# Kernel tuning notes

Measured on AMD Instinct MI355X. Metric: run time of the kernel, lower is better.

Reference implementation:

```python
import jax, jax.numpy as jnp
import numpy as np

N_NODES = 50000
N_EDGES = 800000
IN_F, HID_F, OUT_F = 256, 128, 64


def setup_inputs() -> dict:
    key = jax.random.key(0)
    ks = jax.random.split(key, 9)
    glorot = lambda k, shp: jax.random.normal(k, shp, jnp.float32) * np.sqrt(2.0 / (shp[0] + shp[1]))
    return {
        "x": jax.random.normal(ks[0], (N_NODES, IN_F), jnp.float32),
        "W1": glorot(ks[1], (IN_F, HID_F)),
        "b1": jnp.zeros((HID_F,), jnp.float32),
        "W2": glorot(ks[2], (HID_F, OUT_F)),
        "b2": jnp.zeros((OUT_F,), jnp.float32),
        "Wf": glorot(ks[3], (OUT_F, 2)),
        "bf": jnp.zeros((2,), jnp.float32),
        "src": jax.random.randint(ks[4], (N_EDGES,), 0, N_NODES, jnp.int32),
        "dst": jax.random.randint(ks[5], (N_EDGES,), 0, N_NODES, jnp.int32),
    }


def _gcn_layer(x, src, dst, W, b):
    # DGL GraphConv, norm='both': h = D_in^{-1/2} A D_out^{-1/2} (x W) + b
    n = x.shape[0]
    ones = jnp.ones((src.shape[0],), x.dtype)
    deg_out = jnp.clip(jax.ops.segment_sum(ones, src, num_segments=n), 1.0)
    deg_in = jnp.clip(jax.ops.segment_sum(ones, dst, num_segments=n), 1.0)
    h = x @ W  # transform first (in_feats >= out_feats), cheaper messages
    h = h * jax.lax.rsqrt(deg_out)[:, None]
    agg = jax.ops.segment_sum(h[src], dst, num_segments=n)  # [N, F] sparse aggregate
    return agg * jax.lax.rsqrt(deg_in)[:, None] + b


def reference(x, W1, b1, W2, b2, Wf, bf, src, dst):
    h1 = jax.nn.relu(_gcn_layer(x, src, dst, W1, b1))
    hidden = _gcn_layer(h1, src, dst, W2, b2)
    logits = hidden @ Wf + bf
    return (logits, hidden)
```

## Files before the change

### kernel.cpp

```cpp
#include <hip/hip_runtime.h>
#include <hip/hip_bf16.h>
#include <cstdint>
#include <cstddef>

#define NNODES 50000
#define NEDGES 800000
#define NCH    256
#define CHUNK1 3136
#define NBUCK  196
#define GB1    782
#define SHB    64
#define SHE    12500
#define SHEV   (SHE / 1024)
#define PBN    256
#define PBR    196

typedef unsigned short u16;
typedef unsigned int u32;
typedef short bfrag8 __attribute__((ext_vector_type(8)));
typedef float f32x4 __attribute__((ext_vector_type(4)));

__device__ __forceinline__ u16 f2bf(float f) {
    union { float f; uint32_t i; } v; v.f = f;
    uint32_t r = (v.i + 0x7FFFu + ((v.i >> 16) & 1u)) >> 16;
    return (u16)r;
}
__device__ __forceinline__ float bflo(u32 p) { union { uint32_t i; float f; } v; v.i = p << 16; return v.f; }
__device__ __forceinline__ float bfhi(u32 p) { union { uint32_t i; float f; } v; v.i = p & 0xFFFF0000u; return v.f; }

__global__ __launch_bounds__(256) void pre_kernel(const float* __restrict__ W1, const float* __restrict__ W2,
                                                  u16* __restrict__ P1, u16* __restrict__ P2,
                                                  const int* __restrict__ src, const int* __restrict__ dst,
                                                  u32* __restrict__ histS, u32* __restrict__ histD,
                                                  u32* __restrict__ gh1, int nE) {
    __shared__ u32 hh[12500];
    int b = blockIdx.x, t = threadIdx.x;
    if (b < 2 * SHB) {
        const int* col = (b < SHB) ? src : dst;
        int bb = (b < SHB) ? b : b - SHB;
        for (int j = t; j < 12500; j += 256) hh[j] = 0;
        __syncthreads();
        int beg = bb * SHE;
        const uint4* col4 = (const uint4*)(col + beg);
        #pragma unroll 4
        for (int k = 0; k < SHEV; k++) {
            uint4 e = col4[k * 256 + t];
            atomicAdd(&hh[e.x >> 2], 1u << ((e.x & 3) * 8));
            atomicAdd(&hh[e.y >> 2], 1u << ((e.y & 3) * 8));
            atomicAdd(&hh[e.z >> 2], 1u << ((e.z & 3) * 8));
            atomicAdd(&hh[e.w >> 2], 1u << ((e.w & 3) * 8));
        }
        for (int i = beg + SHEV * 1024 + t; i < beg + SHE; i += 256) {
            u32 n = (u32)col[i];
            atomicAdd(&hh[n >> 2], 1u << ((n & 3) * 8));
        }
        __syncthreads();
        u32* out = ((b < SHB) ? histS : histD) + (size_t)bb * 12500;
        for (int j = t; j < 12500; j += 256) out[j] = hh[j];
    } else if (b < 2 * SHB + NCH) {
        int c = b - 2 * SHB;
        hh[t] = 0;
        __syncthreads();
        int beg = c * CHUNK1, end = min(beg + CHUNK1, nE);
        const uint4* d4 = (const uint4*)(dst + beg);
        int n4 = (end - beg) >> 2;
        for (int k = t; k < n4; k += 256) {
            uint4 e = d4[k];
            atomicAdd(&hh[e.x >> 8], 1u);
            atomicAdd(&hh[e.y >> 8], 1u);
            atomicAdd(&hh[e.z >> 8], 1u);
            atomicAdd(&hh[e.w >> 8], 1u);
        }
        __syncthreads();
        gh1[t * NCH + c] = hh[t];
    } else {
        int i = (b - 2 * SHB - NCH) * 256 + t;
        if (i < 256 * 128) {
            int k = i >> 7, n = i & 127;
            P1[((((k >> 3) << 7) + n) << 3) | (k & 7)] = f2bf(W1[i]);
        }
        if (i < 128 * 64) {
            int k = i >> 6, n = i & 63;
            P2[((((k >> 3) << 6) + n) << 3) | (k & 7)] = f2bf(W2[i]);
        }
    }
}

__global__ __launch_bounds__(256) void red_scan1(const u32* __restrict__ histS, const u32* __restrict__ histD,
                                                 int* __restrict__ deg_out, int* __restrict__ deg_in,
                                                 const u32* __restrict__ gh1, int* __restrict__ scan1,
                                                 int* __restrict__ part1, int* __restrict__ gdh) {
    int t = threadIdx.x, b = blockIdx.x;
    __shared__ int sd[256];
    __shared__ int cnt64[64];
    if (t < 64) cnt64[t] = 0;
    int gi = b * NCH + t;
    int v = (int)gh1[gi];
    sd[t] = v;
    __syncthreads();
    #pragma unroll
    for (int o = 1; o < 256; o <<= 1) {
        int add = (t >= o) ? sd[t - o] : 0;
        __syncthreads();
        sd[t] += add;
        __syncthreads();
    }
    scan1[gi] = sd[t];
    if (t == 255) part1[b] = sd[255];
    int n = b * PBR + t;
    if (t < PBR && n < NNODES) {
        int w = n >> 2, sh = (n & 3) * 8;
        int so = 0, si = 0;
        #pragma unroll 8
        for (int r = 0; r < SHB; r++) {
            so += (int)((histS[(size_t)r * 12500 + w] >> sh) & 255u);
            si += (int)((histD[(size_t)r * 12500 + w] >> sh) & 255u);
        }
        deg_out[n] = so;
        deg_in[n] = si;
        atomicAdd(&cnt64[si > 63 ? 63 : si], 1);
    }
    __syncthreads();
    if (t < 64) gdh[b * 64 + t] = cnt64[t];
}

__global__ __launch_bounds__(256) void scatter1(const int* __restrict__ dst, const int* __restrict__ src,
                                                const u32* __restrict__ gh1, const int* __restrict__ scan1,
                                                const int* __restrict__ part1, u32* __restrict__ sbuf,
                                                const int* __restrict__ gdh, int* __restrict__ gbase, int nE) {
    int t = threadIdx.x, c = blockIdx.x;
    if (c == NCH) {
        __shared__ int colsum[64];
        if (t < 64) {
            int s = 0;
            for (int pb = 0; pb < PBN; pb++) s += gdh[pb * 64 + t];
            colsum[t] = s;
        }
        __syncthreads();
        if (t == 0) {
            int s = 0;
            for (int d = 0; d < 64; d++) { int c0 = colsum[d]; colsum[d] = s; s += c0; }
        }
        __syncthreads();
        if (t < 64) {
            int s = colsum[t];
            for (int pb = 0; pb < PBN; pb++) { gbase[pb * 64 + t] = s; s += gdh[pb * 64 + t]; }
        }
        return;
    }
    __shared__ int sd[256];
    __shared__ int offs[256];
    __shared__ u32 base[256];
    __shared__ u32 lh[256];
    int v = part1[t];
    sd[t] = v;
    __syncthreads();
    #pragma unroll
    for (int o = 1; o < 256; o <<= 1) {
        int add = (t >= o) ? sd[t - o] : 0;
        __syncthreads();
        sd[t] += add;
        __syncthreads();
    }
    offs[t] = sd[t] - v;
    __syncthreads();
    base[t] = (u32)(scan1[t * NCH + c] + offs[t] - (int)gh1[t * NCH + c]);
    lh[t] = 0;
    __syncthreads();
    int beg = c * CHUNK1, end = min(beg + CHUNK1, nE);
    const uint4* s4 = (const uint4*)(src + beg);
    const uint4* d4 = (const uint4*)(dst + beg);
    int n4 = (end - beg) >> 2;
    for (int k = t; k < n4; k += 256) {
        uint4 es = s4[k], ed = d4[k];
        u32 el, dg, r;
        el = (ed.x << 16) | es.x; dg = el >> 24; r = atomicAdd(&lh[dg], 1); sbuf[base[dg] + r] = el;
        el = (ed.y << 16) | es.y; dg = el >> 24; r = atomicAdd(&lh[dg], 1); sbuf[base[dg] + r] = el;
        el = (ed.z << 16) | es.z; dg = el >> 24; r = atomicAdd(&lh[dg], 1); sbuf[base[dg] + r] = el;
        el = (ed.w << 16) | es.w; dg = el >> 24; r = atomicAdd(&lh[dg], 1); sbuf[base[dg] + r] = el;
    }
}

template <int K, int N, bool AF32>
__device__ __forceinline__ void gemm_body(const void* __restrict__ A_, const u16* __restrict__ Wp,
                                          const int* __restrict__ deg, u16* __restrict__ out, int M, int bx) {
    const int lane = threadIdx.x & 63;
    const int wave = threadIdx.x >> 6;
    const int m = lane & 15;
    const int q = lane >> 4;
    const int row0 = bx * 64 + wave * 16;

    int rowa = row0 + m; if (rowa > M - 1) rowa = M - 1;

    constexpr int NT = N / 16;
    f32x4 acc[NT];
    #pragma unroll
    for (int t = 0; t < NT; t++) acc[t] = (f32x4){0.f, 0.f, 0.f, 0.f};

    #pragma unroll
    for (int kc = 0; kc < K; kc += 32) {
        bfrag8 af;
        if constexpr (AF32) {
            const float* ap = (const float*)A_ + (size_t)rowa * K + q * 8 + kc;
            const float4 x0 = *(const float4*)(ap);
            const float4 x1 = *(const float4*)(ap + 4);
            af[0] = (short)f2bf(x0.x); af[1] = (short)f2bf(x0.y);
            af[2] = (short)f2bf(x0.z); af[3] = (short)f2bf(x0.w);
            af[4] = (short)f2bf(x1.x); af[5] = (short)f2bf(x1.y);
            af[6] = (short)f2bf(x1.z); af[7] = (short)f2bf(x1.w);
        } else {
            const u16* ap = (const u16*)A_ + (size_t)rowa * K + q * 8 + kc;
            af = *(const bfrag8*)ap;
        }
        const u16* bbase = Wp + ((size_t)(((kc >> 3) + q) * N) + m) * 8;
        #pragma unroll
        for (int t = 0; t < NT; t++) {
            bfrag8 bf_ = *(const bfrag8*)(bbase + t * 128);
            acc[t] = __builtin_amdgcn_mfma_f32_16x16x32_bf16(af, bf_, acc[t], 0, 0, 0);
        }
    }
    #pragma unroll
    for (int r = 0; r < 4; r++) {
        int gr = row0 + q * 4 + r;
        if (gr < M) {
            int dO = deg[gr]; if (dO < 1) dO = 1;
            float s = rsqrtf((float)dO);
            #pragma unroll
            for (int t = 0; t < NT; t++)
                out[(size_t)gr * N + t * 16 + m] = f2bf(acc[t][r] * s);
        }
    }
}

template <int K, int N, bool AF32>
__global__ __launch_bounds__(256) void gemm_scaled(const void* __restrict__ A_, const u16* __restrict__ Wp,
                                                   const int* __restrict__ deg, u16* __restrict__ out, int M) {
    gemm_body<K, N, AF32>(A_, Wp, deg, out, M, blockIdx.x);
}

__global__ __launch_bounds__(256) void sort_gemm(const u32* __restrict__ sbuf, const int* __restrict__ part1,
                                                 u32* __restrict__ sorted, int* __restrict__ rp,
                                                 const float* __restrict__ x, const u16* __restrict__ Wp1,
                                                 const int* __restrict__ deg_out, const int* __restrict__ deg_in,
                                                 const int* __restrict__ gbase, int* __restrict__ perm,
                                                 u16* __restrict__ h, int nE) {
    int b = blockIdx.x, t = threadIdx.x;
    if (b < NBUCK) {
        __shared__ int sd[256];
        __shared__ int cnt[256];
        __shared__ int cursor[256];
        int v = part1[t];
        sd[t] = v;
        __syncthreads();
        #pragma unroll
        for (int o = 1; o < 256; o <<= 1) {
            int add = (t >= o) ? sd[t - o] : 0;
            __syncthreads();
            sd[t] += add;
            __syncthreads();
        }
        __shared__ int bs_s, bl_s;
        if (t == b) { bs_s = sd[t] - v; bl_s = v; }
        __syncthreads();
        int bstart = bs_s, bend = bstart + bl_s;
        cnt[t] = 0;
        __syncthreads();
        for (int i = bstart + t; i < bend; i += 256)
            atomicAdd(&cnt[(sbuf[i] >> 16) & 255u], 1);
        __syncthreads();
        int cv = cnt[t];
        sd[t] = cv;
        __syncthreads();
        #pragma unroll
        for (int o = 1; o < 256; o <<= 1) {
            int add = (t >= o) ? sd[t - o] : 0;
            __syncthreads();
            sd[t] += add;
            __syncthreads();
        }
        int excl = sd[t] - cv;
        int node = b * 256 + t;
        if (node < NNODES) rp[node] = bstart + excl;
        if (b == NBUCK - 1 && t == 0) rp[NNODES] = nE;
        cursor[t] = excl;
        __syncthreads();
        for (int i = bstart + t; i < bend; i += 256) {
            u32 el = sbuf[i];
            int r = atomicAdd(&cursor[(el >> 16) & 255u], 1);
            sorted[bstart + r] = el;
        }
    } else if (b < NBUCK + GB1) {
        gemm_body<256, 128, true>(x, Wp1, deg_out, h, NNODES, b - NBUCK);
    } else {
        int pb = b - NBUCK - GB1;
        __shared__ int cur[64];
        if (t < 64) cur[t] = gbase[pb * 64 + t];
        __syncthreads();
        int n = pb * PBR + t;
        if (t < PBR && n < NNODES) {
            int d = deg_in[n]; d = d > 63 ? 63 : d;
            int p = atomicAdd(&cur[d], 1);
            perm[p] = n;
        }
    }
}

__global__ __launch_bounds__(256) void gather1f(const uint4* __restrict__ h, const int* __restrict__ row_ptr,
                                                const u32* __restrict__ sorted, const float* __restrict__ b1,
                                                const int* __restrict__ perm, const int* __restrict__ deg_out,
                                                const u16* __restrict__ Wp2, u16* __restrict__ h2) {
    __shared__ __align__(16) u16 sh[16 * 136];
    int t = threadIdx.x;
    int qw = t >> 4;
    int l = t & 15;
    int g = blockIdx.x * 16 + qw;
    int node = perm[g];
    int beg = row_ptr[node], end = row_ptr[node + 1];
    float a[8] = {0.f, 0.f, 0.f, 0.f, 0.f, 0.f, 0.f, 0.f};
    for (int e = beg; e < end; e += 8) {
        uint4 p[8];
        #pragma unroll
        for (int j = 0; j < 8; j++) {
            int ee = e + j; ee = (ee < end - 1) ? ee : end - 1;
            p[j] = h[(size_t)(sorted[ee] & 0xFFFFu) * 16 + l];
        }
        #pragma unroll
        for (int j = 0; j < 8; j++)
            if (e + j < end) {
                a[0] += bflo(p[j].x); a[1] += bfhi(p[j].x);
                a[2] += bflo(p[j].y); a[3] += bfhi(p[j].y);
                a[4] += bflo(p[j].z); a[5] += bfhi(p[j].z);
                a[6] += bflo(p[j].w); a[7] += bfhi(p[j].w);
            }
    }
    int dI = end - beg; if (dI < 1) dI = 1;
    float r = rsqrtf((float)dI);
    const float4 bA = *(const float4*)(b1 + 8 * l);
    const float4 bB = *(const float4*)(b1 + 8 * l + 4);
    float v0 = fmaxf(a[0] * r + bA.x, 0.f), v1 = fmaxf(a[1] * r + bA.y, 0.f);
    float v2 = fmaxf(a[2] * r + bA.z, 0.f), v3 = fmaxf(a[3] * r + bA.w, 0.f);
    float v4 = fmaxf(a[4] * r + bB.x, 0.f), v5 = fmaxf(a[5] * r + bB.y, 0.f);
    float v6 = fmaxf(a[6] * r + bB.z, 0.f), v7 = fmaxf(a[7] * r + bB.w, 0.f);
    uint4 o;
    o.x = ((u32)f2bf(v1) << 16) | f2bf(v0);
    o.y = ((u32)f2bf(v3) << 16) | f2bf(v2);
    o.z = ((u32)f2bf(v5) << 16) | f2bf(v4);
    o.w = ((u32)f2bf(v7) << 16) | f2bf(v6);
    *(uint4*)&sh[qw * 136 + l * 8] = o;
    __syncthreads();
    const int lane = t & 63;
    const int m = lane & 15;
    const int q = lane >> 4;
    const int w = t >> 6;
    f32x4 acc = (f32x4){0.f, 0.f, 0.f, 0.f};
    #pragma unroll
    for (int kc = 0; kc < 128; kc += 32) {
        bfrag8 af = *(const bfrag8*)&sh[m * 136 + q * 8 + kc];
        bfrag8 bf_ = *(const bfrag8*)(Wp2 + ((size_t)(((kc >> 3) + q) * 64) + w * 16 + m) * 8);
        acc = __builtin_amdgcn_mfma_f32_16x16x32_bf16(af, bf_, acc, 0, 0, 0);
    }
    #pragma unroll
    for (int rr = 0; rr < 4; rr++) {
        int li = q * 4 + rr;
        int nd = perm[blockIdx.x * 16 + li];
        int dO = deg_out[nd]; if (dO < 1) dO = 1;
        float s = rsqrtf((float)dO);
        h2[(size_t)nd * 64 + w * 16 + m] = f2bf(acc[rr] * s);
    }
}

__global__ __launch_bounds__(256) void gather2(const uint4* __restrict__ h2, const int* __restrict__ row_ptr,
                                               const u32* __restrict__ sorted, const float* __restrict__ b2,
                                               const float* __restrict__ Wf, const float* __restrict__ bfv,
                                               const int* __restrict__ perm,
                                               float* __restrict__ logits, float* __restrict__ hidden, int nNodes) {
    int g = (blockIdx.x * 256 + threadIdx.x) >> 3;
    int l = threadIdx.x & 7;
    if (g >= nNodes) return;
    int node = perm[g];
    int beg = row_ptr[node], end = row_ptr[node + 1];
    float a[8] = {0.f, 0.f, 0.f, 0.f, 0.f, 0.f, 0.f, 0.f};
    for (int e = beg; e < end; e += 8) {
        uint4 p[8];
        #pragma unroll
        for (int j = 0; j < 8; j++) {
            int ee = e + j; ee = (ee < end - 1) ? ee : end - 1;
            p[j] = h2[(size_t)(sorted[ee] & 0xFFFFu) * 8 + l];
        }
        #pragma unroll
        for (int j = 0; j < 8; j++)
            if (e + j < end) {
                a[0] += bflo(p[j].x); a[1] += bfhi(p[j].x);
                a[2] += bflo(p[j].y); a[3] += bfhi(p[j].y);
                a[4] += bflo(p[j].z); a[5] += bfhi(p[j].z);
                a[6] += bflo(p[j].w); a[7] += bfhi(p[j].w);
            }
    }
    int dI = end - beg; if (dI < 1) dI = 1;
    float r = rsqrtf((float)dI);
    float v[8];
    #pragma unroll
    for (int f = 0; f < 8; f++) v[f] = a[f] * r + b2[8 * l + f];
    float4 oA = {v[0], v[1], v[2], v[3]};
    float4 oB = {v[4], v[5], v[6], v[7]};
    ((float4*)hidden)[(size_t)node * 16 + 2 * l + 0] = oA;
    ((float4*)hidden)[(size_t)node * 16 + 2 * l + 1] = oB;
    float l0 = 0.f, l1 = 0.f;
    #pragma unroll
    for (int f = 0; f < 8; f++) {
        l0 += v[f] * Wf[(8 * l + f) * 2 + 0];
        l1 += v[f] * Wf[(8 * l + f) * 2 + 1];
    }
    #pragma unroll
    for (int off = 4; off > 0; off >>= 1) {
        l0 += __shfl_down(l0, off, 8);
        l1 += __shfl_down(l1, off, 8);
    }
    if (l == 0) {
        logits[(size_t)node * 2 + 0] = l0 + bfv[0];
        logits[(size_t)node * 2 + 1] = l1 + bfv[1];
    }
}

extern "C" void kernel_launch(void* const* d_in, const int* in_sizes, int n_in,
                              void* d_out, int out_size, void* d_ws, size_t ws_size,
                              hipStream_t stream) {
    const float* x   = (const float*)d_in[0];
    const float* W1  = (const float*)d_in[1];
    const float* b1  = (const float*)d_in[2];
    const float* W2  = (const float*)d_in[3];
    const float* b2  = (const float*)d_in[4];
    const float* Wf  = (const float*)d_in[5];
    const float* bfv = (const float*)d_in[6];
    const int* src = (const int*)d_in[7];
    const int* dst = (const int*)d_in[8];

    float* out_logits = (float*)d_out;
    float* out_hidden = (float*)d_out + 2 * NNODES;

    char* ws = (char*)d_ws;
    size_t off = 0;
    auto alloc = [&](size_t bytes) { void* p = ws + off; off += (bytes + 255) & ~(size_t)255; return p; };
    u32*   gh1     = (u32*)alloc(NCH * NCH * 4);
    int*   scan1   = (int*)alloc(NCH * NCH * 4);
    int*   part1   = (int*)alloc(256 * 4);
    u32*   sbuf    = (u32*)alloc((size_t)NEDGES * 4);
    u32*   sorted  = (u32*)alloc((size_t)NEDGES * 4);
    u32*   histS   = (u32*)alloc((size_t)SHB * 12500 * 4);
    u32*   histD   = (u32*)alloc((size_t)SHB * 12500 * 4);
    int*   deg     = (int*)alloc(2 * NNODES * 4);
    int*   row_ptr = (int*)alloc((NNODES + 1) * 4);
    int*   gdh     = (int*)alloc(PBN * 64 * 4);
    int*   gbase   = (int*)alloc(PBN * 64 * 4);
    int*   perm    = (int*)alloc(NNODES * 4);
    u16*   Wp1     = (u16*)alloc(256 * 128 * 2);
    u16*   Wp2     = (u16*)alloc(128 * 64 * 2);
    u16*   h       = (u16*)alloc((size_t)NNODES * 128 * 2);
    u16*   h2      = (u16*)alloc((size_t)NNODES * 64 * 2);

    int* deg_out = deg;
    int* deg_in  = deg + NNODES;

    pre_kernel<<<2 * SHB + NCH + 128, 256, 0, stream>>>(W1, W2, Wp1, Wp2, src, dst, histS, histD, gh1, NEDGES);
    red_scan1<<<NCH, 256, 0, stream>>>(histS, histD, deg_out, deg_in, gh1, scan1, part1, gdh);
    scatter1<<<NCH + 1, 256, 0, stream>>>(dst, src, gh1, scan1, part1, sbuf, gdh, gbase, NEDGES);
    sort_gemm<<<NBUCK + GB1 + PBN, 256, 0, stream>>>(sbuf, part1, sorted, row_ptr, x, Wp1,
                                                     deg_out, deg_in, gbase, perm, h, NEDGES);
    gather1f<<<NNODES / 16, 256, 0, stream>>>((const uint4*)h, row_ptr, sorted, b1, perm, deg_out, Wp2, h2);
    gather2<<<(NNODES * 8 + 255) / 256, 256, 0, stream>>>((const uint4*)h2, row_ptr, sorted, b2, Wf, bfv,
                                                          perm, out_logits, out_hidden, NNODES);
}
```

Baseline: 195.8 us.

## Merge scan and scatter kernels, recompute prefix sums redundantly per block

Fuses red_scan1 and scatter1 into one kernel. Each block recomputes its bucket totals and column prefixes directly from a transposed u16 histogram instead of reading a separately scanned array, and the degree-bucket base offsets are recomputed inside the sort_gemm perm blocks rather than by a dedicated block. This drops one kernel launch and its global round trip of scan data. The cost is redundant reads of the 256x256 histogram in every block and a serial 256-iteration loop per perm block.

```diff
diff --git a/kernel.cpp b/kernel.cpp
--- a/kernel.cpp
+++ b/kernel.cpp
@@ -32,7 +32,7 @@
                                                   u16* __restrict__ P1, u16* __restrict__ P2,
                                                   const int* __restrict__ src, const int* __restrict__ dst,
                                                   u32* __restrict__ histS, u32* __restrict__ histD,
-                                                  u32* __restrict__ gh1, int nE) {
+                                                  u16* __restrict__ gh1, int nE) {
     __shared__ u32 hh[12500];
     int b = blockIdx.x, t = threadIdx.x;
     if (b < 2 * SHB) {
@@ -72,7 +72,7 @@
             atomicAdd(&hh[e.w >> 8], 1u);
         }
         __syncthreads();
-        gh1[t * NCH + c] = hh[t];
+        gh1[c * NCH + t] = (u16)hh[t];
     } else {
         int i = (b - 2 * SHB - NCH) * 256 + t;
         if (i < 256 * 128) {
@@ -86,17 +86,27 @@
     }
 }
 
-__global__ __launch_bounds__(256) void red_scan1(const u32* __restrict__ histS, const u32* __restrict__ histD,
-                                                 int* __restrict__ deg_out, int* __restrict__ deg_in,
-                                                 const u32* __restrict__ gh1, int* __restrict__ scan1,
-                                                 int* __restrict__ part1, int* __restrict__ gdh) {
-    int t = threadIdx.x, b = blockIdx.x;
+__global__ __launch_bounds__(256) void scat_deg(const int* __restrict__ src, const int* __restrict__ dst,
+                                                const u16* __restrict__ gh1,
+                                                const u32* __restrict__ histS, const u32* __restrict__ histD,
+                                                int* __restrict__ deg_out, int* __restrict__ deg_in,
+                                                int* __restrict__ gdh, int* __restrict__ part1,
+                                                u32* __restrict__ sbuf, int nE) {
+    int t = threadIdx.x, c = blockIdx.x;
     __shared__ int sd[256];
+    __shared__ u32 base[256];
+    __shared__ u32 lh[256];
     __shared__ int cnt64[64];
     if (t < 64) cnt64[t] = 0;
-    int gi = b * NCH + t;
-    int v = (int)gh1[gi];
-    sd[t] = v;
+    int tot = 0, par = 0;
+    #pragma unroll 8
+    for (int cc = 0; cc < NCH; cc++) {
+        int v = (int)gh1[cc * NCH + t];
+        tot += v;
+        par += (cc < c) ? v : 0;
+    }
+    if (c == 0) part1[t] = tot;
+    sd[t] = tot;
     __syncthreads();
     #pragma unroll
     for (int o = 1; o < 256; o <<= 1) {
@@ -105,66 +115,7 @@
         sd[t] += add;
         __syncthreads();
     }
-    scan1[gi] = sd[t];
-    if (t == 255) part1[b] = sd[255];
-    int n = b * PBR + t;
-    if (t < PBR && n < NNODES) {
-        int w = n >> 2, sh = (n & 3) * 8;
-        int so = 0, si = 0;
-        #pragma unroll 8
-        for (int r = 0; r < SHB; r++) {
-            so += (int)((histS[(size_t)r * 12500 + w] >> sh) & 255u);
-            si += (int)((histD[(size_t)r * 12500 + w] >> sh) & 255u);
-        }
-        deg_out[n] = so;
-        deg_in[n] = si;
-        atomicAdd(&cnt64[si > 63 ? 63 : si], 1);
-    }
-    __syncthreads();
-    if (t < 64) gdh[b * 64 + t] = cnt64[t];
-}
-
-__global__ __launch_bounds__(256) void scatter1(const int* __restrict__ dst, const int* __restrict__ src,
-                                                const u32* __restrict__ gh1, const int* __restrict__ scan1,
-                                                const int* __restrict__ part1, u32* __restrict__ sbuf,
-                                                const int* __restrict__ gdh, int* __restrict__ gbase, int nE) {
-    int t = threadIdx.x, c = blockIdx.x;
-    if (c == NCH) {
-        __shared__ int colsum[64];
-        if (t < 64) {
-            int s = 0;
-            for (int pb = 0; pb < PBN; pb++) s += gdh[pb * 64 + t];
-            colsum[t] = s;
-        }
-        __syncthreads();
-        if (t == 0) {
-            int s = 0;
-            for (int d = 0; d < 64; d++) { int c0 = colsum[d]; colsum[d] = s; s += c0; }
-        }
-        __syncthreads();
-        if (t < 64) {
-            int s = colsum[t];
-            for (int pb = 0; pb < PBN; pb++) { gbase[pb * 64 + t] = s; s += gdh[pb * 64 + t]; }
-        }
-        return;
-    }
-    __shared__ int sd[256];
-    __shared__ int offs[256];
-    __shared__ u32 base[256];
-    __shared__ u32 lh[256];
-    int v = part1[t];
-    sd[t] = v;
-    __syncthreads();
-    #pragma unroll
-    for (int o = 1; o < 256; o <<= 1) {
-        int add = (t >= o) ? sd[t - o] : 0;
-        __syncthreads();
-        sd[t] += add;
-        __syncthreads();
-    }
-    offs[t] = sd[t] - v;
-    __syncthreads();
-    base[t] = (u32)(scan1[t * NCH + c] + offs[t] - (int)gh1[t * NCH + c]);
+    base[t] = (u32)((sd[t] - tot) + par);
     lh[t] = 0;
     __syncthreads();
     int beg = c * CHUNK1, end = min(beg + CHUNK1, nE);
@@ -179,6 +130,21 @@
         el = (ed.z << 16) | es.z; dg = el >> 24; r = atomicAdd(&lh[dg], 1); sbuf[base[dg] + r] = el;
         el = (ed.w << 16) | es.w; dg = el >> 24; r = atomicAdd(&lh[dg], 1); sbuf[base[dg] + r] = el;
     }
+    int n = c * PBR + t;
+    if (t < PBR && n < NNODES) {
+        int w = n >> 2, sh = (n & 3) * 8;
+        int so = 0, si = 0;
+        #pragma unroll 8
+        for (int r = 0; r < SHB; r++) {
+            so += (int)((histS[(size_t)r * 12500 + w] >> sh) & 255u);
+            si += (int)((histD[(size_t)r * 12500 + w] >> sh) & 255u);
+        }
+        deg_out[n] = so;
+        deg_in[n] = si;
+        atomicAdd(&cnt64[si > 63 ? 63 : si], 1);
+    }
+    __syncthreads();
+    if (t < 64) gdh[c * 64 + t] = cnt64[t];
 }
 
 template <int K, int N, bool AF32>
@@ -232,17 +198,11 @@
     }
 }
 
-template <int K, int N, bool AF32>
-__global__ __launch_bounds__(256) void gemm_scaled(const void* __restrict__ A_, const u16* __restrict__ Wp,
-                                                   const int* __restrict__ deg, u16* __restrict__ out, int M) {
-    gemm_body<K, N, AF32>(A_, Wp, deg, out, M, blockIdx.x);
-}
-
 __global__ __launch_bounds__(256) void sort_gemm(const u32* __restrict__ sbuf, const int* __restrict__ part1,
                                                  u32* __restrict__ sorted, int* __restrict__ rp,
                                                  const float* __restrict__ x, const u16* __restrict__ Wp1,
                                                  const int* __restrict__ deg_out, const int* __restrict__ deg_in,
-                                                 const int* __restrict__ gbase, int* __restrict__ perm,
+                                                 const int* __restrict__ gdh, int* __restrict__ perm,
                                                  u16* __restrict__ h, int nE) {
     int b = blockIdx.x, t = threadIdx.x;
     if (b < NBUCK) {
@@ -293,8 +253,25 @@
         gemm_body<256, 128, true>(x, Wp1, deg_out, h, NNODES, b - NBUCK);
     } else {
         int pb = b - NBUCK - GB1;
+        __shared__ int cse[64];
         __shared__ int cur[64];
-        if (t < 64) cur[t] = gbase[pb * 64 + t];
+        if (t < 64) {
+            int s_all = 0, s_pre = 0;
+            for (int q2 = 0; q2 < PBN; q2++) {
+                int v = gdh[q2 * 64 + t];
+                s_all += v;
+                s_pre += (q2 < pb) ? v : 0;
+            }
+            cse[t] = s_all;
+            cur[t] = s_pre;
+        }
+        __syncthreads();
+        if (t == 0) {
+            int s = 0;
+            for (int d2 = 0; d2 < 64; d2++) { int v = cse[d2]; cse[d2] = s; s += v; }
+        }
+        __syncthreads();
+        if (t < 64) cur[t] += cse[t];
         __syncthreads();
         int n = pb * PBR + t;
         if (t < PBR && n < NNODES) {
@@ -441,8 +418,7 @@
     char* ws = (char*)d_ws;
     size_t off = 0;
     auto alloc = [&](size_t bytes) { void* p = ws + off; off += (bytes + 255) & ~(size_t)255; return p; };
-    u32*   gh1     = (u32*)alloc(NCH * NCH * 4);
-    int*   scan1   = (int*)alloc(NCH * NCH * 4);
+    u16*   gh1     = (u16*)alloc(NCH * NCH * 2);
     int*   part1   = (int*)alloc(256 * 4);
     u32*   sbuf    = (u32*)alloc((size_t)NEDGES * 4);
     u32*   sorted  = (u32*)alloc((size_t)NEDGES * 4);
@@ -451,7 +427,6 @@
     int*   deg     = (int*)alloc(2 * NNODES * 4);
     int*   row_ptr = (int*)alloc((NNODES + 1) * 4);
     int*   gdh     = (int*)alloc(PBN * 64 * 4);
-    int*   gbase   = (int*)alloc(PBN * 64 * 4);
     int*   perm    = (int*)alloc(NNODES * 4);
     u16*   Wp1     = (u16*)alloc(256 * 128 * 2);
     u16*   Wp2     = (u16*)alloc(128 * 64 * 2);
@@ -462,10 +437,9 @@
     int* deg_in  = deg + NNODES;
 
     pre_kernel<<<2 * SHB + NCH + 128, 256, 0, stream>>>(W1, W2, Wp1, Wp2, src, dst, histS, histD, gh1, NEDGES);
-    red_scan1<<<NCH, 256, 0, stream>>>(histS, histD, deg_out, deg_in, gh1, scan1, part1, gdh);
-    scatter1<<<NCH + 1, 256, 0, stream>>>(dst, src, gh1, scan1, part1, sbuf, gdh, gbase, NEDGES);
+    scat_deg<<<NCH, 256, 0, stream>>>(src, dst, gh1, histS, histD, deg_out, deg_in, gdh, part1, sbuf, NEDGES);
     sort_gemm<<<NBUCK + GB1 + PBN, 256, 0, stream>>>(sbuf, part1, sorted, row_ptr, x, Wp1,
-                                                     deg_out, deg_in, gbase, perm, h, NEDGES);
+                                                     deg_out, deg_in, gdh, perm, h, NEDGES);
     gather1f<<<NNODES / 16, 256, 0, stream>>>((const uint4*)h, row_ptr, sorted, b1, perm, deg_out, Wp2, h2);
     gather2<<<(NNODES * 8 + 255) / 256, 256, 0, stream>>>((const uint4*)h2, row_ptr, sorted, b2, Wf, bfv,
                                                           perm, out_logits, out_hidden, NNODES);
```

Result: no change. 193.8 us (-1.0%).
